# Kernel optimization log

Hardware: AMD Instinct MI355X
Metric: run time of the kernel (lower is better)

The kernel has to match this reference:

```python
import jax, jax.numpy as jnp
from jax import lax
import numpy as np

N = 20000        # nodes
E = 160000       # directed edges (doubled to 2E inside forward)
NODE_DIM = 6
EDGE_DIM = 4
HID = 64         # hidden_dim
HEADS = 4
ITERS = 3
D_OUT = HEADS * HID          # 256
SQRT_D = 8.0                 # sqrt(HID)
ALLOWED = jnp.array([8., 23., 39., 54., 90., 180.], dtype=jnp.float32)


def _ln(x, g, b):
    m = jnp.mean(x, -1, keepdims=True)
    v = jnp.mean((x - m) ** 2, -1, keepdims=True)
    return (x - m) * lax.rsqrt(v + 1e-5) * g + b


def _cbam(x, w1, b1, w2, b2, cw, cb):
    # channel attention: pool over nodes (dim 0)
    pool = jnp.concatenate([x.max(0, keepdims=True), x.mean(0, keepdims=True)], axis=1)  # [1,2D]
    ch = jax.nn.sigmoid(jnp.maximum(pool @ w1 + b1, 0.) @ w2 + b2)                        # [1,D]
    x = x * ch
    # spatial attention: pool over features, conv1d over node axis
    cat = jnp.concatenate([x.max(-1, keepdims=True), x.mean(-1, keepdims=True)], axis=-1)  # [N,2]
    inp = cat.T[None]                                                                       # [1,2,N]
    sp = lax.conv_general_dilated(inp, cw, (1,), [(3, 3)],
                                  dimension_numbers=('NCH', 'OIH', 'NCH')) + cb[None, :, None]
    return x * jax.nn.sigmoid(sp)[0, 0][:, None]


def _tconv(xc, src, dst, wq, b_q, wk, b_k, wv, b_v, ws, b_s):
    # PyG TransformerConv (concat=True, root_weight=True, no edge features)
    n = xc.shape[0]
    q = (xc @ wq + b_q).reshape(n, HEADS, HID)
    k = (xc @ wk + b_k).reshape(n, HEADS, HID)
    v = (xc @ wv + b_v).reshape(n, HEADS, HID)
    alpha = jnp.einsum('ehd,ehd->eh', q[dst], k[src]) / SQRT_D           # [2E,H]
    amax = jax.ops.segment_max(alpha, dst, num_segments=n)
    a = jnp.exp(alpha - amax[dst])
    a = a / jax.ops.segment_sum(a, dst, num_segments=n)[dst]
    out = jax.ops.segment_sum(a[..., None] * v[src], dst, num_segments=n).reshape(n, D_OUT)
    return out + xc @ ws + b_s


def reference(x, edge_attr, node_w, node_b, edge_w, edge_b, z_emb,
              cn_w1, cn_b1, cn_w2, cn_b2, cn_cw, cn_cb,
              ce_w1, ce_b1, ce_w2, ce_b2, ce_cw, ce_cb,
              Wq, bq, Wk, bk, Wv, bv, Ws, bs,
              lt_g, lt_b, lc_g, lc_b,
              pe_w, pe_b, pn_w, pn_b, gf_w, gf_b,
              c_w1, c_b1, c_w2, c_b2, edge_index):
    send = jnp.concatenate([edge_index[0], edge_index[1]])
    recv = jnp.concatenate([edge_index[1], edge_index[0]])
    src, dst = send, recv                                           # [2E]
    rel = x[src, :3] - x[dst, :3]                                   # [2E,3]
    zi = jnp.argmin(jnp.abs(jnp.round(x[:, 2])[:, None] - ALLOWED[None, :]), axis=1)
    nf = jnp.maximum(x @ node_w + node_b, 0.) + z_emb[zi]           # node embedding + z embedding
    nf = _cbam(nf, cn_w1, cn_b1, cn_w2, cn_b2, cn_cw, cn_cb)
    ef = jnp.concatenate([jnp.concatenate([edge_attr, edge_attr], 0), rel], axis=1)
    ef = jnp.maximum(ef @ edge_w + edge_b, 0.)
    ef = _cbam(ef, ce_w1, ce_b1, ce_w2, ce_b2, ce_cw, ce_cb)
    n = nf.shape[0]
    for i in range(ITERS):
        x0, e0 = nf, ef
        agg = jax.ops.segment_sum(ef, dst, num_segments=n)          # scatter-add messages
        comb = _ln(jnp.concatenate([nf, agg - nf], 1), lc_g[i], lc_b[i])
        out = _tconv(comb, src, dst, Wq[i], bq[i], Wk[i], bk[i], Wv[i], bv[i], Ws[i], bs[i])
        out = _ln(out, lt_g[i], lt_b[i])
        pn = out @ pn_w[i] + pn_b[i]
        g = jax.nn.sigmoid(jnp.concatenate([nf, pn], 1) @ gf_w[i] + gf_b[i])  # gated fusion
        nf = nf * g + pn * (1. - g)
        ef = (out[src] - out[dst]) @ pe_w[i] + pe_b[i]
        nf = nf + x0
        ef = ef + e0
    clf = jnp.concatenate([nf[edge_index[0]], nf[edge_index[1]]], axis=1)
    h = jnp.maximum(clf @ c_w1 + c_b1, 0.)
    return (h @ c_w2 + c_b2)[:, 0]


def setup_inputs() -> dict:
    key = jax.random.key(0)
    ki = iter(jax.random.split(key, 64))
    def rn(shape, s=0.05):
        return jax.random.normal(next(ki), shape, dtype=jnp.float32) * s
    x = jax.random.normal(next(ki), (N, NODE_DIM), dtype=jnp.float32)
    x = x.at[:, 2].set(ALLOWED[jax.random.randint(next(ki), (N,), 0, 6)])
    inp = {
        'x': x,
        'edge_attr': jax.random.normal(next(ki), (E, EDGE_DIM), dtype=jnp.float32),
        'node_w': rn((NODE_DIM, HID)), 'node_b': jnp.zeros(HID),
        'edge_w': rn((EDGE_DIM + 3, HID)), 'edge_b': jnp.zeros(HID),
        'z_emb': rn((6, HID)),
        'cn_w1': rn((2 * HID, HID // 16)), 'cn_b1': jnp.zeros(HID // 16),
        'cn_w2': rn((HID // 16, HID)), 'cn_b2': jnp.zeros(HID),
        'cn_cw': rn((1, 2, 7)), 'cn_cb': jnp.zeros(1),
        'ce_w1': rn((2 * HID, HID // 16)), 'ce_b1': jnp.zeros(HID // 16),
        'ce_w2': rn((HID // 16, HID)), 'ce_b2': jnp.zeros(HID),
        'ce_cw': rn((1, 2, 7)), 'ce_cb': jnp.zeros(1),
        'Wq': rn((ITERS, 2 * HID, D_OUT)), 'bq': jnp.zeros((ITERS, D_OUT)),
        'Wk': rn((ITERS, 2 * HID, D_OUT)), 'bk': jnp.zeros((ITERS, D_OUT)),
        'Wv': rn((ITERS, 2 * HID, D_OUT)), 'bv': jnp.zeros((ITERS, D_OUT)),
        'Ws': rn((ITERS, 2 * HID, D_OUT)), 'bs': jnp.zeros((ITERS, D_OUT)),
        'lt_g': jnp.ones((ITERS, D_OUT)), 'lt_b': jnp.zeros((ITERS, D_OUT)),
        'lc_g': jnp.ones((ITERS, 2 * HID)), 'lc_b': jnp.zeros((ITERS, 2 * HID)),
        'pe_w': rn((ITERS, D_OUT, HID)), 'pe_b': jnp.zeros((ITERS, HID)),
        'pn_w': rn((ITERS, D_OUT, HID)), 'pn_b': jnp.zeros((ITERS, HID)),
        'gf_w': rn((ITERS, 2 * HID, HID)), 'gf_b': jnp.zeros((ITERS, HID)),
        'c_w1': rn((2 * HID, HID)), 'c_b1': jnp.zeros(HID),
        'c_w2': rn((HID, 1)), 'c_b2': jnp.zeros(1),
        'edge_index': jax.random.randint(next(ki), (2, E), 0, N),
    }
    return inp
```

## Files before the change

kernel.cpp:

```cpp
#include <hip/hip_runtime.h>
#include <math.h>

typedef __attribute__((ext_vector_type(8))) short short8;
typedef __attribute__((ext_vector_type(4))) float f32x4;

__device__ __forceinline__ float wave_sum(float v){
  #pragma unroll
  for (int m = 32; m; m >>= 1) v += __shfl_xor(v, m, 64);
  return v;
}
__device__ __forceinline__ unsigned fenc(float f){
  unsigned u = __float_as_uint(f);
  return (u >> 31) ? ~u : (u | 0x80000000u);
}
__device__ __forceinline__ float fdec(unsigned e){
  return (e >> 31) ? __uint_as_float(e & 0x7fffffffu) : __uint_as_float(~e);
}
__device__ __forceinline__ float sigm(float x){ return 1.f / (1.f + __expf(-x)); }
__device__ __forceinline__ unsigned short f2bf(float f){
  union { float f; unsigned u; } x; x.f = f;
  unsigned r = x.u + 0x7fffu + ((x.u >> 16) & 1u);
  return (unsigned short)(r >> 16);
}
__device__ __forceinline__ float bf2f(unsigned short h){
  union { unsigned u; float f; } x; x.u = ((unsigned)h) << 16;
  return x.f;
}

__global__ void k_build_edges(const int* __restrict__ ei, int E2, int E,
                              int* __restrict__ src, int* __restrict__ dst,
                              int* __restrict__ deg){
  int e = blockIdx.x * blockDim.x + threadIdx.x;
  if (e >= E2) return;
  int s = ei[e];
  int d = (e < E) ? ei[e + E] : ei[e - E];
  src[e] = s; dst[e] = d;
  atomicAdd(&deg[d], 1);
}

__global__ void k_scan(const int* __restrict__ deg, int* __restrict__ rowptr, int N){
  __shared__ int part[1024];
  int t = threadIdx.x;
  int chunk = (N + 1023) / 1024;
  int lo = t * chunk, hi = lo + chunk; if (hi > N) hi = N;
  int s = 0;
  for (int i = lo; i < hi; ++i) s += deg[i];
  part[t] = s;
  __syncthreads();
  for (int off = 1; off < 1024; off <<= 1){
    int v = (t >= off) ? part[t - off] : 0;
    __syncthreads();
    part[t] += v;
    __syncthreads();
  }
  int run = part[t] - s;
  for (int i = lo; i < hi; ++i){ rowptr[i] = run; run += deg[i]; }
  if (t == 1023) rowptr[N] = part[1023];
}

__global__ void k_fill(const int* __restrict__ src, const int* __restrict__ dst,
                       const int* __restrict__ rowptr,
                       int* __restrict__ cur, int* __restrict__ csrc,
                       int* __restrict__ epos,
                       const float* __restrict__ x, const float* __restrict__ ea,
                       float* __restrict__ re8, int E2, int E){
  int e = blockIdx.x * blockDim.x + threadIdx.x;
  if (e >= E2) return;
  int s = src[e], d = dst[e];
  int pos = rowptr[d] + atomicAdd(&cur[d], 1);
  csrc[pos] = s;
  epos[e] = pos;
  int row = (e < E) ? e : e - E;
  float4 eav = *reinterpret_cast<const float4*>(ea + (size_t)row*4);
  float r0 = x[s*6]     - x[d*6];
  float r1 = x[s*6 + 1] - x[d*6 + 1];
  float r2 = x[s*6 + 2] - x[d*6 + 2];
  *reinterpret_cast<float4*>(re8 + (size_t)e*8)     = eav;
  *reinterpret_cast<float4*>(re8 + (size_t)e*8 + 4) = make_float4(r0, r1, r2, 0.f);
}

__global__ void k_embed_pool(const float* __restrict__ x, const float* __restrict__ nw,
                             const float* __restrict__ nb, const float* __restrict__ zemb,
                             float* __restrict__ nf,
                             unsigned* __restrict__ pmax, float* __restrict__ psum, int N){
  int tx = threadIdx.x & 63;
  int ty = threadIdx.x >> 6;
  const float allowed[6] = {8.f, 23.f, 39.f, 54.f, 90.f, 180.f};
  float m = -INFINITY, s = 0.f;
  for (int n = blockIdx.x*4 + ty; n < N; n += gridDim.x*4){
    float xv[6];
    #pragma unroll
    for (int k = 0; k < 6; ++k) xv[k] = x[n*6 + k];
    float v = nb[tx];
    #pragma unroll
    for (int k = 0; k < 6; ++k) v += xv[k] * nw[k*64 + tx];
    v = fmaxf(v, 0.f);
    float r = rintf(xv[2]);
    int zi = 0; float bd = fabsf(r - allowed[0]);
    #pragma unroll
    for (int k = 1; k < 6; ++k){ float d = fabsf(r - allowed[k]); if (d < bd){ bd = d; zi = k; } }
    v += zemb[zi*64 + tx];
    nf[(size_t)n*64 + tx] = v;
    m = fmaxf(m, v); s += v;
  }
  __shared__ float sm[4][64], ss[4][64];
  sm[ty][tx] = m; ss[ty][tx] = s;
  __syncthreads();
  if (ty == 0){
    #pragma unroll
    for (int k = 1; k < 4; ++k){ m = fmaxf(m, sm[k][tx]); s += ss[k][tx]; }
    atomicMax(&pmax[tx], fenc(m));
    atomicAdd(&psum[tx], s);
  }
}

__global__ void k_cbam_mlp(const unsigned* __restrict__ pmax, const float* __restrict__ psum,
                           float invR,
                           const float* __restrict__ w1, const float* __restrict__ b1,
                           const float* __restrict__ w2, const float* __restrict__ b2,
                           float* __restrict__ ch){
  __shared__ float pool[128];
  __shared__ float h[4];
  int t = threadIdx.x;
  pool[t]      = fdec(pmax[t]);
  pool[64 + t] = psum[t] * invR;
  __syncthreads();
  if (t < 4){
    float a = b1[t];
    for (int k = 0; k < 128; ++k) a += pool[k] * w1[k*4 + t];
    h[t] = fmaxf(a, 0.f);
  }
  __syncthreads();
  float a = b2[t];
  #pragma unroll
  for (int k = 0; k < 4; ++k) a += h[k] * w2[k*64 + t];
  ch[t] = sigm(a);
}

__global__ __launch_bounds__(256) void k_nsp(
    float* __restrict__ nf, const float* __restrict__ ch,
    const float* __restrict__ cw, const float* __restrict__ cb,
    unsigned short* __restrict__ gin, int N){
  __shared__ float s_v[134*65];
  __shared__ float s_rp[134][2];
  int tid = threadIdx.x;
  int tx = tid & 63, wv = tid >> 6;
  float chl = ch[tx];
  int base = blockIdx.x * 128;
  for (int li = wv; li < 134; li += 4){
    int r = base - 3 + li;
    if (r >= 0 && r < N)
      s_v[li*65 + tx] = nf[(size_t)r*64 + tx] * chl;
  }
  __syncthreads();
  #pragma unroll
  for (int pass = 0; pass < 2; ++pass){
    int li = (tid >> 1) + pass*128;
    if (li < 134){
      int r = base - 3 + li;
      if (r >= 0 && r < N){
        const float* vb = &s_v[li*65 + (tid & 1)*32];
        float m = vb[0], s = vb[0];
        #pragma unroll 8
        for (int k = 1; k < 32; ++k){ float t = vb[k]; m = fmaxf(m, t); s += t; }
        float mo = __shfl_xor(m, 1, 64);
        float so = __shfl_xor(s, 1, 64);
        m = fmaxf(m, mo); s += so;
        if ((tid & 1) == 0){ s_rp[li][0] = m; s_rp[li][1] = s * (1.f/64.f); }
      }
    }
  }
  __syncthreads();
  for (int li = 3 + wv; li < 131; li += 4){
    int r = base - 3 + li;
    if (r >= N) continue;
    float sp = cb[0];
    #pragma unroll
    for (int t7 = 0; t7 < 7; ++t7){
      int rr = r + t7 - 3;
      if (rr >= 0 && rr < N)
        sp += cw[t7] * s_rp[li - 3 + t7][0] + cw[7 + t7] * s_rp[li - 3 + t7][1];
    }
    float nfv = s_v[li*65 + tx] * sigm(sp);
    nf[(size_t)r*64 + tx] = nfv;
    gin[(size_t)r*128 + tx] = f2bf(nfv);
  }
}

__global__ __launch_bounds__(256) void k_ecol(
    const float* __restrict__ re8,
    const float* __restrict__ ew, const float* __restrict__ eb,
    unsigned* __restrict__ pmax, float* __restrict__ psum, int E2){
  __shared__ float s_re[2][1024];
  int tid = threadIdx.x;
  int tx = tid & 63, wv = tid >> 6;
  float ewr[7];
  #pragma unroll
  for (int k = 0; k < 7; ++k) ewr[k] = ew[k*64 + tx];
  float ebl = eb[tx];
  const int CHUNK = 128;
  int base0  = blockIdx.x * CHUNK;
  int stride = gridDim.x * CHUNK;
  float m = -INFINITY, s = 0.f;
  if (base0 < E2){
    int g0 = base0 * 8;
    #pragma unroll
    for (int q = 0; q < 4; ++q){
      int idx = q*256 + tid;
      int gi = g0 + idx;
      s_re[0][idx] = (gi < E2*8) ? re8[gi] : 0.f;
    }
  }
  int buf = 0;
  for (int base = base0; base < E2; base += stride){
    __syncthreads();
    int nb = base + stride;
    if (nb < E2){
      int g0 = nb * 8;
      #pragma unroll
      for (int q = 0; q < 4; ++q){
        int idx = q*256 + tid;
        int gi = g0 + idx;
        s_re[buf ^ 1][idx] = (gi < E2*8) ? re8[gi] : 0.f;
      }
    }
    const float* sb = s_re[buf];
    #pragma unroll
    for (int j = 0; j < 32; ++j){
      int e = base + wv*32 + j;
      if (e < E2){
        const float* r = &sb[(wv*32 + j)*8];
        float v = ebl;
        #pragma unroll
        for (int k = 0; k < 7; ++k) v += r[k] * ewr[k];
        v = fmaxf(v, 0.f);
        m = fmaxf(m, v); s += v;
      }
    }
    buf ^= 1;
  }
  __shared__ float sm[4][64], ss[4][64];
  sm[wv][tx] = m; ss[wv][tx] = s;
  __syncthreads();
  if (wv == 0){
    #pragma unroll
    for (int k = 1; k < 4; ++k){ m = fmaxf(m, sm[k][tx]); s += ss[k][tx]; }
    atomicMax(&pmax[tx], fenc(m));
    atomicAdd(&psum[tx], s);
  }
}

__global__ __launch_bounds__(256) void k_erp3(
    const float* __restrict__ re8, const int* __restrict__ epos,
    const float* __restrict__ ew, const float* __restrict__ eb,
    const float* __restrict__ ch,
    const float* __restrict__ ccw, const float* __restrict__ ccb,
    unsigned short* __restrict__ ef0, float* __restrict__ se, int E2){
  __shared__ float s_re[134*8];
  __shared__ float s_v[134*65];
  __shared__ float s_rp[134][2];
  __shared__ int   s_ep[128];
  int tid = threadIdx.x;
  int tx = tid & 63, wv = tid >> 6;
  float ewr[7];
  #pragma unroll
  for (int k = 0; k < 7; ++k) ewr[k] = ew[k*64 + tx];
  float ebl = eb[tx], chl = ch[tx];
  int base = blockIdx.x * 128;
  for (int idx = tid; idx < 134*8; idx += 256){
    int li = idx >> 3, k = idx & 7;
    int e = base - 3 + li;
    s_re[idx] = (e >= 0 && e < E2) ? re8[(size_t)e*8 + k] : 0.f;
  }
  if (tid < 128 && base + tid < E2) s_ep[tid] = epos[base + tid];
  __syncthreads();
  for (int li = wv; li < 134; li += 4){
    int e = base - 3 + li;
    if (e < 0 || e >= E2) continue;
    const float* r = &s_re[li*8];
    float v = ebl;
    #pragma unroll
    for (int k = 0; k < 7; ++k) v += r[k] * ewr[k];
    v = fmaxf(v, 0.f) * chl;
    s_v[li*65 + tx] = v;
    if (li >= 3 && li < 131)
      ef0[(size_t)s_ep[li - 3]*64 + tx] = f2bf(v);
  }
  __syncthreads();
  #pragma unroll
  for (int pass = 0; pass < 2; ++pass){
    int li = (tid >> 1) + pass*128;
    if (li < 134){
      int e = base - 3 + li;
      if (e >= 0 && e < E2){
        const float* vb = &s_v[li*65 + (tid & 1)*32];
        float m = vb[0], s = vb[0];
        #pragma unroll 8
        for (int k = 1; k < 32; ++k){ float t = vb[k]; m = fmaxf(m, t); s += t; }
        float mo = __shfl_xor(m, 1, 64);
        float so = __shfl_xor(s, 1, 64);
        m = fmaxf(m, mo); s += so;
        if ((tid & 1) == 0){ s_rp[li][0] = m; s_rp[li][1] = s * (1.f/64.f); }
      }
    }
  }
  __syncthreads();
  if (tid < 128){
    int e = base + tid;
    if (e < E2){
      float sp = ccb[0];
      #pragma unroll
      for (int t7 = 0; t7 < 7; ++t7){
        int rr = e + t7 - 3;
        if (rr >= 0 && rr < E2)
          sp += ccw[t7] * s_rp[tid + t7][0] + ccw[7 + t7] * s_rp[tid + t7][1];
      }
      se[s_ep[tid]] = sigm(sp);
    }
  }
}

__global__ void k_aggb(const unsigned short* __restrict__ ef0, const float* __restrict__ se,
                       const int* __restrict__ rowptr, const float* __restrict__ nf,
                       const float* __restrict__ g, const float* __restrict__ b,
                       float* __restrict__ agg, unsigned short* __restrict__ comb, int N){
  int n = blockIdx.x*4 + (threadIdx.x >> 6);
  if (n >= N) return;
  int l = threadIdx.x & 63;
  int lo = rowptr[n], hi = rowptr[n+1];
  float acc = 0.f;
  int i = lo;
  for (; i + 8 <= hi; i += 8){
    float sv[8], ev[8];
    #pragma unroll
    for (int j = 0; j < 8; ++j) sv[j] = se[i + j];
    #pragma unroll
    for (int j = 0; j < 8; ++j) ev[j] = bf2f(ef0[(size_t)(i + j)*64 + l]);
    #pragma unroll
    for (int j = 0; j < 8; ++j) acc += sv[j] * ev[j];
  }
  for (; i < hi; ++i) acc += se[i] * bf2f(ef0[(size_t)i*64 + l]);
  agg[(size_t)n*64 + l] = acc;
  float a = nf[(size_t)n*64 + l];
  float v0 = a, v1 = acc - a;
  float mean = wave_sum(v0 + v1) * (1.f/128.f);
  float d0 = v0 - mean, d1 = v1 - mean;
  float var = wave_sum(d0*d0 + d1*d1) * (1.f/128.f);
  float rs = rsqrtf(var + 1e-5f);
  comb[(size_t)n*128 + l]      = f2bf(d0 * rs * g[l]      + b[l]);
  comb[(size_t)n*128 + 64 + l] = f2bf(d1 * rs * g[64 + l] + b[64 + l]);
}

__global__ __launch_bounds__(256) void k_packT1(
    const float* __restrict__ Wq, const float* __restrict__ Wk,
    const float* __restrict__ Wv, const float* __restrict__ Ws,
    unsigned short* __restrict__ Bt){
  __shared__ float t[64][65];
  int bx = blockIdx.x, by = blockIdx.y, bz = blockIdx.z;
  const float* W = (bz == 0) ? Wq : (bz == 1) ? Wk : (bz == 2) ? Wv : Ws;
  int tx = threadIdx.x & 63, ty = threadIdx.x >> 6;
  int R0 = by*64, C0 = bx*64;
  for (int r = ty; r < 64; r += 4)
    t[r][tx] = W[(size_t)(R0 + r)*256 + C0 + tx];
  __syncthreads();
  int iter = by >> 1, kr0 = (by & 1)*64;
  for (int r = ty; r < 64; r += 4)
    Bt[(size_t)iter*1024*128 + (size_t)(bz*256 + C0 + r)*128 + kr0 + tx] = f2bf(t[tx][r]);
}

__global__ __launch_bounds__(256) void k_packT2(
    const float* __restrict__ Wn, const float* __restrict__ We,
    unsigned short* __restrict__ Bt2){
  __shared__ float t[64][65];
  int by = blockIdx.y, bz = blockIdx.z;
  const float* W = (bz == 0) ? Wn : We;
  int tx = threadIdx.x & 63, ty = threadIdx.x >> 6;
  int R0 = by*64;
  for (int r = ty; r < 64; r += 4)
    t[r][tx] = W[(size_t)(R0 + r)*64 + tx];
  __syncthreads();
  int iter = by >> 2, kr0 = (by & 3)*64;
  for (int r = ty; r < 64; r += 4)
    Bt2[(size_t)iter*128*256 + (size_t)(bz*64 + r)*256 + kr0 + tx] = f2bf(t[tx][r]);
}

__global__ void k_packG(const float* __restrict__ gfw, unsigned short* __restrict__ BtG){
  int b = blockIdx.x;
  int iter = b >> 7, col = b & 127;
  int k = threadIdx.x;
  unsigned short v = 0;
  if (col < 64) v = f2bf(gfw[(size_t)iter*128*64 + (size_t)k*64 + col]);
  BtG[(size_t)b*128 + k] = v;
}

__global__ void k_biasp(const float* __restrict__ bq, const float* __restrict__ bk,
                        const float* __restrict__ bv, const float* __restrict__ bs,
                        const float* __restrict__ pnb, const float* __restrict__ gfb,
                        float* __restrict__ bias, float* __restrict__ bias2,
                        float* __restrict__ bias3){
  int i = blockIdx.x, t = threadIdx.x;
  const float* bb = (t < 256) ? bq : (t < 512) ? bk : (t < 768) ? bv : bs;
  bias[i*1024 + t] = bb[i*256 + (t & 255)];
  if (t < 64){
    bias2[i*128 + t] = pnb[i*64 + t];
    bias3[i*128 + t] = gfb[i*64 + t];
  } else if (t < 128){
    bias2[i*128 + t] = 0.f;
    bias3[i*128 + t] = 0.f;
  }
}

__global__ void k_packC(const float* __restrict__ cw1, float* __restrict__ Wp){
  int idx = blockIdx.x * blockDim.x + threadIdx.x;
  if (idx >= 64*128) return;
  int k = idx >> 7, j = idx & 127;
  Wp[idx] = (j < 64) ? cw1[k*64 + j] : cw1[(64 + k)*64 + (j - 64)];
}

template<int NSTEPS, int MODE>
__global__ __launch_bounds__(256) void k_mfma(
    const unsigned short* __restrict__ A, int lda,
    const unsigned short* __restrict__ Bt, int ldb,
    const float* __restrict__ bias,
    float* __restrict__ o_f0, unsigned short* __restrict__ o_h0,
    unsigned short* __restrict__ o_h1, int M){
  __shared__ char ldsA[16384];
  int tid = threadIdx.x;
  int nbase = blockIdx.x * 128;
  int mbase = blockIdx.y * 64;
  int l = tid & 63, wid = tid >> 6;
  int wm = (wid & 1) * 32, wn = (wid >> 1) * 64;
  f32x4 acc[2][4] = {};
  const char* Ab  = (const char*)A;
  const char* Btb = (const char*)Bt;
  for (int ks = 0; ks < NSTEPS; ++ks){
    #pragma unroll
    for (int it = 0; it < 4; ++it){
      int c = tid + it*256;
      int row = c >> 4;
      int kb = (c & 15) << 4;
      int off = (row << 8) + (kb ^ ((row & 7) << 4));
      uint4 va = make_uint4(0,0,0,0);
      int gr = mbase + row;
      if (gr < M)
        va = *reinterpret_cast<const uint4*>(Ab + (size_t)gr*(lda*2) + ks*256 + kb);
      *reinterpret_cast<uint4*>(ldsA + off) = va;
    }
    __syncthreads();
    #pragma unroll
    for (int kk = 0; kk < 4; ++kk){
      int kbyte = kk*64 + (l >> 4)*16;
      short8 af[2], bf[4];
      #pragma unroll
      for (int n = 0; n < 4; ++n){
        int fc = wn + n*16 + (l & 15);
        bf[n] = *reinterpret_cast<const short8*>(
                  Btb + (size_t)(nbase + fc)*(ldb*2) + ks*256 + kbyte);
      }
      #pragma unroll
      for (int m = 0; m < 2; ++m){
        int fr = wm + m*16 + (l & 15);
        af[m] = *reinterpret_cast<const short8*>(ldsA + (fr << 8) + (kbyte ^ ((fr & 7) << 4)));
      }
      #pragma unroll
      for (int m = 0; m < 2; ++m)
        #pragma unroll
        for (int n = 0; n < 4; ++n)
          acc[m][n] = __builtin_amdgcn_mfma_f32_16x16x32_bf16(af[m], bf[n], acc[m][n], 0, 0, 0);
    }
    __syncthreads();
  }
  #pragma unroll
  for (int n = 0; n < 4; ++n){
    int gcol = nbase + wn + n*16 + (l & 15);
    float bv = bias ? bias[gcol] : 0.f;
    #pragma unroll
    for (int m = 0; m < 2; ++m){
      int grow = mbase + wm + m*16 + (l >> 4)*4;
      #pragma unroll
      for (int r = 0; r < 4; ++r){
        int gr = grow + r;
        if (gr < M){
          float val = acc[m][n][r] + bv;
          if (MODE == 1){
            o_f0[(size_t)gr*128 + gcol] = val;
            if (gcol < 64) o_h0[(size_t)gr*128 + 64 + gcol] = f2bf(val);
          } else if (MODE == 2){
            if (gcol < 64) o_f0[(size_t)gr*64 + gcol] = val;
          } else {
            int seg = gcol >> 8, c = gcol & 255;
            if      (seg == 0) o_h1[(size_t)gr*512 + c] = f2bf(val);
            else if (seg == 1) o_h0[(size_t)gr*512 + c] = f2bf(val);
            else if (seg == 2) o_h0[(size_t)gr*512 + 256 + c] = f2bf(val);
            else               o_h1[(size_t)gr*512 + 256 + c] = f2bf(val);
          }
        }
      }
    }
  }
}

__global__ void k_attn(const unsigned short* __restrict__ qs,
                       const unsigned short* __restrict__ kv,
                       const int* __restrict__ rowptr, const int* __restrict__ csrc,
                       const float* __restrict__ ltg, const float* __restrict__ ltb,
                       unsigned short* __restrict__ outb, int N){
  int n = blockIdx.x*4 + (threadIdx.x >> 6);
  if (n >= N) return;
  int l = threadIdx.x & 63;
  int lo = rowptr[n], hi = rowptr[n+1];
  const int l4 = l*4;
  ushort4 qu = *reinterpret_cast<const ushort4*>(qs + (size_t)n*512 + l4);
  float4 qv = make_float4(bf2f(qu.x)*0.125f, bf2f(qu.y)*0.125f,
                          bf2f(qu.z)*0.125f, bf2f(qu.w)*0.125f);
  float o0 = 0.f, o1 = 0.f, o2 = 0.f, o3 = 0.f, s = 0.f;
  int i = lo;
  for (; i + 16 <= hi; i += 16){
    ushort4 kk[16], vv[16];
    #pragma unroll
    for (int j = 0; j < 16; ++j){
      const unsigned short* row = kv + (size_t)csrc[i + j]*512 + l4;
      kk[j] = *reinterpret_cast<const ushort4*>(row);
      vv[j] = *reinterpret_cast<const ushort4*>(row + 256);
    }
    float a[16];
    #pragma unroll
    for (int j = 0; j < 16; ++j)
      a[j] = qv.x*bf2f(kk[j].x) + qv.y*bf2f(kk[j].y) + qv.z*bf2f(kk[j].z) + qv.w*bf2f(kk[j].w);
    #pragma unroll
    for (int m = 1; m < 16; m <<= 1){
      #pragma unroll
      for (int j = 0; j < 16; ++j) a[j] += __shfl_xor(a[j], m, 64);
    }
    #pragma unroll
    for (int j = 0; j < 16; ++j){
      float w = __expf(a[j]);
      s += w;
      o0 += w*bf2f(vv[j].x); o1 += w*bf2f(vv[j].y);
      o2 += w*bf2f(vv[j].z); o3 += w*bf2f(vv[j].w);
    }
  }
  for (; i + 8 <= hi; i += 8){
    ushort4 kk[8], vv[8];
    #pragma unroll
    for (int j = 0; j < 8; ++j){
      const unsigned short* row = kv + (size_t)csrc[i + j]*512 + l4;
      kk[j] = *reinterpret_cast<const ushort4*>(row);
      vv[j] = *reinterpret_cast<const ushort4*>(row + 256);
    }
    float a[8];
    #pragma unroll
    for (int j = 0; j < 8; ++j)
      a[j] = qv.x*bf2f(kk[j].x) + qv.y*bf2f(kk[j].y) + qv.z*bf2f(kk[j].z) + qv.w*bf2f(kk[j].w);
    #pragma unroll
    for (int m = 1; m < 16; m <<= 1){
      #pragma unroll
      for (int j = 0; j < 8; ++j) a[j] += __shfl_xor(a[j], m, 64);
    }
    #pragma unroll
    for (int j = 0; j < 8; ++j){
      float w = __expf(a[j]);
      s += w;
      o0 += w*bf2f(vv[j].x); o1 += w*bf2f(vv[j].y);
      o2 += w*bf2f(vv[j].z); o3 += w*bf2f(vv[j].w);
    }
  }
  for (; i < hi; ++i){
    const unsigned short* row = kv + (size_t)csrc[i]*512 + l4;
    ushort4 kk = *reinterpret_cast<const ushort4*>(row);
    ushort4 vv = *reinterpret_cast<const ushort4*>(row + 256);
    float a = qv.x*bf2f(kk.x) + qv.y*bf2f(kk.y) + qv.z*bf2f(kk.z) + qv.w*bf2f(kk.w);
    #pragma unroll
    for (int m = 1; m < 16; m <<= 1) a += __shfl_xor(a, m, 64);
    float w = __expf(a);
    s += w;
    o0 += w*bf2f(vv.x); o1 += w*bf2f(vv.y); o2 += w*bf2f(vv.z); o3 += w*bf2f(vv.w);
  }
  ushort4 su = *reinterpret_cast<const ushort4*>(qs + (size_t)n*512 + 256 + l4);
  float tx0 = bf2f(su.x), tx1 = bf2f(su.y), tx2 = bf2f(su.z), tx3 = bf2f(su.w);
  if (hi > lo){
    float r = 1.f / s;
    tx0 += o0*r; tx1 += o1*r; tx2 += o2*r; tx3 += o3*r;
  }
  float mean = wave_sum(tx0 + tx1 + tx2 + tx3) * (1.f/256.f);
  float dx = tx0 - mean, dy = tx1 - mean, dz = tx2 - mean, dw = tx3 - mean;
  float var = wave_sum(dx*dx + dy*dy + dz*dz + dw*dw) * (1.f/256.f);
  float rs = rsqrtf(var + 1e-5f);
  float4 g = *reinterpret_cast<const float4*>(ltg + l4);
  float4 b = *reinterpret_cast<const float4*>(ltb + l4);
  ushort4 o;
  o.x = f2bf(dx*rs*g.x + b.x);
  o.y = f2bf(dy*rs*g.y + b.y);
  o.z = f2bf(dz*rs*g.z + b.z);
  o.w = f2bf(dw*rs*g.w + b.w);
  *reinterpret_cast<ushort4*>(outb + (size_t)n*256 + l4) = o;
}

__global__ __launch_bounds__(256) void k_gate2(
    float* __restrict__ nf, float* __restrict__ agg,
    const float* __restrict__ pnP, const float* __restrict__ gate_arg,
    const int* __restrict__ rowptr, const int* __restrict__ csrc,
    const float* __restrict__ peb,
    const float* __restrict__ cg, const float* __restrict__ cbv,
    unsigned short* __restrict__ comb, unsigned short* __restrict__ gin,
    int doComb, int N){
  int n = blockIdx.x*4 + (threadIdx.x >> 6);
  if (n >= N) return;
  int l = threadIdx.x & 63;
  float g = sigm(gate_arg[(size_t)n*64 + l]);
  float nfv = nf[(size_t)n*64 + l];
  float pnv = pnP[(size_t)n*128 + l];
  float nfn = nfv * (1.f + g) + pnv * (1.f - g);
  nf[(size_t)n*64 + l] = nfn;
  gin[(size_t)n*128 + l] = f2bf(nfn);
  int lo = rowptr[n], hi = rowptr[n+1];
  float sp = 0.f;
  int i = lo;
  for (; i + 8 <= hi; i += 8){
    float pv[8];
    #pragma unroll
    for (int j = 0; j < 8; ++j)
      pv[j] = pnP[(size_t)csrc[i+j]*128 + 64 + l];
    #pragma unroll
    for (int j = 0; j < 8; ++j) sp += pv[j];
  }
  for (; i < hi; ++i) sp += pnP[(size_t)csrc[i]*128 + 64 + l];
  float Pn = pnP[(size_t)n*128 + 64 + l];
  float aggn = agg[(size_t)n*64 + l] + sp - (float)(hi - lo) * (Pn - peb[l]);
  agg[(size_t)n*64 + l] = aggn;
  if (doComb){
    float v0 = nfn, v1 = aggn - nfn;
    float mean = wave_sum(v0 + v1) * (1.f/128.f);
    float d0 = v0 - mean, d1 = v1 - mean;
    float var = wave_sum(d0*d0 + d1*d1) * (1.f/128.f);
    float rs = rsqrtf(var + 1e-5f);
    comb[(size_t)n*128 + l]      = f2bf(d0 * rs * cg[l]      + cbv[l]);
    comb[(size_t)n*128 + 64 + l] = f2bf(d1 * rs * cg[64 + l] + cbv[64 + l]);
  }
}

template<int K, int BN>
__global__ __launch_bounds__(256) void k_gemm(
    const float* __restrict__ in, const float* __restrict__ W, int ldw,
    const float* __restrict__ bias, float* __restrict__ out, int ldo, int nrows){
  constexpr int PAD = BN + 4;
  __shared__ float s_in[K * PAD];
  int n0 = blockIdx.x * BN;
  int tid = threadIdx.x;
  for (int idx = tid; idx < BN * K; idx += 256){
    int r = idx / K, k = idx - r * K;
    float v = (n0 + r < nrows) ? in[(size_t)(n0 + r) * K + k] : 0.f;
    s_in[k * PAD + r] = v;
  }
  __syncthreads();
  int tx = tid & 15, ty = tid >> 4;
  constexpr int NT = BN / 16;
  int col0 = blockIdx.y * 64 + tx * 4;
  float acc[NT][4] = {};
  for (int k = 0; k < K; ++k){
    const float4 wv = *reinterpret_cast<const float4*>(&W[(size_t)k * ldw + col0]);
    #pragma unroll
    for (int i = 0; i < NT; ++i){
      float cv = s_in[k * PAD + ty * NT + i];
      acc[i][0] += cv * wv.x;
      acc[i][1] += cv * wv.y;
      acc[i][2] += cv * wv.z;
      acc[i][3] += cv * wv.w;
    }
  }
  #pragma unroll
  for (int i = 0; i < NT; ++i){
    int n = n0 + ty * NT + i;
    if (n < nrows){
      float4 o = make_float4(acc[i][0], acc[i][1], acc[i][2], acc[i][3]);
      *reinterpret_cast<float4*>(&out[(size_t)n * ldo + col0]) = o;
    }
  }
}

__global__ void k_final(const float* __restrict__ AB,
                        const int* __restrict__ ei, const float* __restrict__ cb1,
                        const float* __restrict__ cw2, const float* __restrict__ cb2,
                        float* __restrict__ dout, int E){
  int e = blockIdx.x*4 + (threadIdx.x >> 6);
  if (e >= E) return;
  int l = threadIdx.x & 63;
  int i0 = ei[e], i1 = ei[E + e];
  float h = fmaxf(AB[(size_t)i0*128 + l] + AB[(size_t)i1*128 + 64 + l] + cb1[l], 0.f);
  float p = wave_sum(h * cw2[l]);
  if (l == 0) dout[e] = p + cb2[0];
}

extern "C" void kernel_launch(void* const* d_in, const int* in_sizes, int n_in,
                              void* d_out, int out_size, void* d_ws, size_t ws_size,
                              hipStream_t stream){
  const float* x         = (const float*)d_in[0];
  const float* edge_attr = (const float*)d_in[1];
  const float* node_w    = (const float*)d_in[2];
  const float* node_b    = (const float*)d_in[3];
  const float* edge_w    = (const float*)d_in[4];
  const float* edge_b    = (const float*)d_in[5];
  const float* z_emb     = (const float*)d_in[6];
  const float* cn_w1     = (const float*)d_in[7];
  const float* cn_b1     = (const float*)d_in[8];
  const float* cn_w2     = (const float*)d_in[9];
  const float* cn_b2     = (const float*)d_in[10];
  const float* cn_cw     = (const float*)d_in[11];
  const float* cn_cb     = (const float*)d_in[12];
  const float* ce_w1     = (const float*)d_in[13];
  const float* ce_b1     = (const float*)d_in[14];
  const float* ce_w2     = (const float*)d_in[15];
  const float* ce_b2     = (const float*)d_in[16];
  const float* ce_cw     = (const float*)d_in[17];
  const float* ce_cb     = (const float*)d_in[18];
  const float* Wq        = (const float*)d_in[19];
  const float* bq        = (const float*)d_in[20];
  const float* Wk        = (const float*)d_in[21];
  const float* bk        = (const float*)d_in[22];
  const float* Wv        = (const float*)d_in[23];
  const float* bv        = (const float*)d_in[24];
  const float* Ws        = (const float*)d_in[25];
  const float* bs        = (const float*)d_in[26];
  const float* lt_g      = (const float*)d_in[27];
  const float* lt_b      = (const float*)d_in[28];
  const float* lc_g      = (const float*)d_in[29];
  const float* lc_b      = (const float*)d_in[30];
  const float* pe_w      = (const float*)d_in[31];
  const float* pe_b      = (const float*)d_in[32];
  const float* pn_w      = (const float*)d_in[33];
  const float* pn_b      = (const float*)d_in[34];
  const float* gf_w      = (const float*)d_in[35];
  const float* gf_b      = (const float*)d_in[36];
  const float* c_w1      = (const float*)d_in[37];
  const float* c_b1      = (const float*)d_in[38];
  const float* c_w2      = (const float*)d_in[39];
  const float* c_b2      = (const float*)d_in[40];
  const int*   edge_index= (const int*)d_in[41];

  const int N  = in_sizes[0] / 6;
  const int E  = in_sizes[1] / 4;
  const int E2 = 2 * E;

  char* p = (char*)d_ws;
  auto alloc = [&](size_t bytes)->char*{
    char* r = p; p += (bytes + 255) & ~(size_t)255; return r;
  };
  char* zbase = p;
  int*            w_deg    = (int*)           alloc((size_t)N * 4);
  int*            w_cur    = (int*)           alloc((size_t)N * 4);
  unsigned*       w_pmax   = (unsigned*)      alloc(64 * 4);
  float*          w_psum   = (float*)         alloc(64 * 4);
  unsigned*       w_pmax2  = (unsigned*)      alloc(64 * 4);
  float*          w_psum2  = (float*)         alloc(64 * 4);
  size_t zbytes = (size_t)(p - zbase);
  int*            w_src    = (int*)           alloc((size_t)E2 * 4);
  int*            w_dst    = (int*)           alloc((size_t)E2 * 4);
  int*            w_rowptr = (int*)           alloc((size_t)(N + 1) * 4);
  int*            w_csrc   = (int*)           alloc((size_t)E2 * 4);
  int*            w_epos   = (int*)           alloc((size_t)E2 * 4);
  float*          w_re8    = (float*)         alloc((size_t)E2 * 8 * 4);
  float*          w_nf     = (float*)         alloc((size_t)N * 64 * 4);
  float*          w_agg    = (float*)         alloc((size_t)N * 64 * 4);
  unsigned short* w_ef0    = (unsigned short*)alloc((size_t)E2 * 64 * 2);
  float*          w_se     = (float*)         alloc((size_t)E2 * 4);
  unsigned short* w_comb   = (unsigned short*)alloc((size_t)N * 128 * 2);
  unsigned short* w_gin    = (unsigned short*)alloc((size_t)N * 128 * 2);
  float*          w_gate   = (float*)         alloc((size_t)N * 64 * 4);
  unsigned short* w_qs     = (unsigned short*)alloc((size_t)N * 512 * 2);
  unsigned short* w_kv     = (unsigned short*)alloc((size_t)N * 512 * 2);
  unsigned short* w_outb   = (unsigned short*)alloc((size_t)N * 256 * 2);
  float*          w_pnP    = (float*)         alloc((size_t)N * 128 * 4);
  float*          w_AB     = (float*)         alloc((size_t)N * 128 * 4);
  float*          w_Wp     = (float*)         alloc((size_t)64 * 128 * 4);
  unsigned short* w_Bt     = (unsigned short*)alloc((size_t)3 * 1024 * 128 * 2);
  float*          w_bias   = (float*)         alloc((size_t)3 * 1024 * 4);
  unsigned short* w_Bt2    = (unsigned short*)alloc((size_t)3 * 128 * 256 * 2);
  float*          w_bias2  = (float*)         alloc((size_t)3 * 128 * 4);
  unsigned short* w_BtG    = (unsigned short*)alloc((size_t)3 * 128 * 128 * 2);
  float*          w_bias3  = (float*)         alloc((size_t)3 * 128 * 4);
  float*          w_ch     = (float*)         alloc(64 * 4);
  float*          w_ch2    = (float*)         alloc(64 * 4);

  hipMemsetAsync(zbase, 0, zbytes, stream);

  k_build_edges<<<(E2 + 255)/256, 256, 0, stream>>>(edge_index, E2, E, w_src, w_dst, w_deg);
  k_scan<<<1, 1024, 0, stream>>>(w_deg, w_rowptr, N);
  k_fill<<<(E2 + 255)/256, 256, 0, stream>>>(w_src, w_dst, w_rowptr, w_cur, w_csrc, w_epos,
                                             x, edge_attr, w_re8, E2, E);
  k_embed_pool<<<256, 256, 0, stream>>>(x, node_w, node_b, z_emb, w_nf, w_pmax, w_psum, N);
  k_cbam_mlp<<<1, 64, 0, stream>>>(w_pmax, w_psum, 1.f/(float)N,
                                   cn_w1, cn_b1, cn_w2, cn_b2, w_ch);
  k_nsp<<<(N + 127)/128, 256, 0, stream>>>(w_nf, w_ch, cn_cw, cn_cb, w_gin, N);

  k_ecol<<<256, 256, 0, stream>>>(w_re8, edge_w, edge_b, w_pmax2, w_psum2, E2);
  k_cbam_mlp<<<1, 64, 0, stream>>>(w_pmax2, w_psum2, 1.f/(float)E2,
                                   ce_w1, ce_b1, ce_w2, ce_b2, w_ch2);
  k_erp3<<<(E2 + 127)/128, 256, 0, stream>>>(w_re8, w_epos, edge_w, edge_b, w_ch2,
                                             ce_cw, ce_cb, w_ef0, w_se, E2);
  k_aggb<<<(N + 3)/4, 256, 0, stream>>>(w_ef0, w_se, w_rowptr, w_nf,
                                        lc_g, lc_b, w_agg, w_comb, N);

  k_packT1<<<dim3(4, 6, 4), 256, 0, stream>>>(Wq, Wk, Wv, Ws, w_Bt);
  k_packT2<<<dim3(1, 12, 2), 256, 0, stream>>>(pn_w, pe_w, w_Bt2);
  k_packG<<<3*128, 128, 0, stream>>>(gf_w, w_BtG);
  k_biasp<<<3, 1024, 0, stream>>>(bq, bk, bv, bs, pn_b, gf_b, w_bias, w_bias2, w_bias3);
  k_packC<<<32, 256, 0, stream>>>(c_w1, w_Wp);

  const int MB2 = (N + 63) / 64;
  for (int i = 0; i < 3; ++i){
    k_mfma<1,0><<<dim3(8, MB2), 256, 0, stream>>>(w_comb, 128,
                                                  w_Bt + (size_t)i*1024*128, 128,
                                                  w_bias + (size_t)i*1024,
                                                  nullptr, w_kv, w_qs, N);
    k_attn<<<(N + 3)/4, 256, 0, stream>>>(w_qs, w_kv, w_rowptr, w_csrc,
                                          lt_g + (size_t)i*256, lt_b + (size_t)i*256,
                                          w_outb, N);
    k_mfma<2,1><<<dim3(1, MB2), 256, 0, stream>>>(w_outb, 256,
                                                  w_Bt2 + (size_t)i*128*256, 256,
                                                  w_bias2 + (size_t)i*128,
                                                  w_pnP, w_gin, nullptr, N);
    k_mfma<1,2><<<dim3(1, MB2), 256, 0, stream>>>(w_gin, 128,
                                                  w_BtG + (size_t)i*128*128, 128,
                                                  w_bias3 + (size_t)i*128,
                                                  w_gate, nullptr, nullptr, N);
    int doComb = (i < 2) ? 1 : 0;
    const float* cg  = lc_g + (size_t)(i < 2 ? i+1 : 0)*128;
    const float* cbv = lc_b + (size_t)(i < 2 ? i+1 : 0)*128;
    k_gate2<<<(N + 3)/4, 256, 0, stream>>>(w_nf, w_agg, w_pnP, w_gate,
                                           w_rowptr, w_csrc,
                                           pe_b + (size_t)i*64,
                                           cg, cbv, w_comb, w_gin, doComb, N);
  }

  dim3 gAB((N + 63)/64, 2);
  k_gemm<64,64><<<gAB, 256, 0, stream>>>(w_nf, w_Wp, 128, nullptr, w_AB, 128, N);
  k_final<<<(E + 3)/4, 256, 0, stream>>>(w_AB, edge_index, c_b1, c_w2, c_b2,
                                         (float*)d_out, E);
}
```

Measured before the change: 710.4 us.

## Gather neighbor projections from compact bf16 copy; drop 16-edge attention unroll

The MODE 1 GEMM epilogue now also writes the second 64 columns of the projection as a compact bf16 array. The gate kernel's neighbor-sum gather reads that array instead of strided fp32 rows, which cuts gather traffic per edge. Separately, the 16-wide unrolled edge loop in the attention kernel is removed, leaving the 8-wide loop, to lower register pressure and raise occupancy. The bf16 gather adds rounding error to the aggregate, and the smaller unroll has fewer loads in flight per wave.

Measured after the change: 692.1 us. 2.6% less time.

```diff
diff --git a/kernel.cpp b/kernel.cpp
--- a/kernel.cpp
+++ b/kernel.cpp
@@ -485,6 +485,7 @@
           if (MODE == 1){
             o_f0[(size_t)gr*128 + gcol] = val;
             if (gcol < 64) o_h0[(size_t)gr*128 + 64 + gcol] = f2bf(val);
+            else           o_h1[(size_t)gr*64 + (gcol - 64)] = f2bf(val);
           } else if (MODE == 2){
             if (gcol < 64) o_f0[(size_t)gr*64 + gcol] = val;
           } else {
@@ -515,31 +516,6 @@
                           bf2f(qu.z)*0.125f, bf2f(qu.w)*0.125f);
   float o0 = 0.f, o1 = 0.f, o2 = 0.f, o3 = 0.f, s = 0.f;
   int i = lo;
-  for (; i + 16 <= hi; i += 16){
-    ushort4 kk[16], vv[16];
-    #pragma unroll
-    for (int j = 0; j < 16; ++j){
-      const unsigned short* row = kv + (size_t)csrc[i + j]*512 + l4;
-      kk[j] = *reinterpret_cast<const ushort4*>(row);
-      vv[j] = *reinterpret_cast<const ushort4*>(row + 256);
-    }
-    float a[16];
-    #pragma unroll
-    for (int j = 0; j < 16; ++j)
-      a[j] = qv.x*bf2f(kk[j].x) + qv.y*bf2f(kk[j].y) + qv.z*bf2f(kk[j].z) + qv.w*bf2f(kk[j].w);
-    #pragma unroll
-    for (int m = 1; m < 16; m <<= 1){
-      #pragma unroll
-      for (int j = 0; j < 16; ++j) a[j] += __shfl_xor(a[j], m, 64);
-    }
-    #pragma unroll
-    for (int j = 0; j < 16; ++j){
-      float w = __expf(a[j]);
-      s += w;
-      o0 += w*bf2f(vv[j].x); o1 += w*bf2f(vv[j].y);
-      o2 += w*bf2f(vv[j].z); o3 += w*bf2f(vv[j].w);
-    }
-  }
   for (; i + 8 <= hi; i += 8){
     ushort4 kk[8], vv[8];
     #pragma unroll
@@ -598,7 +574,8 @@
 
 __global__ __launch_bounds__(256) void k_gate2(
     float* __restrict__ nf, float* __restrict__ agg,
-    const float* __restrict__ pnP, const float* __restrict__ gate_arg,
+    const float* __restrict__ pnP, const unsigned short* __restrict__ Pbf,
+    const float* __restrict__ gate_arg,
     const int* __restrict__ rowptr, const int* __restrict__ csrc,
     const float* __restrict__ peb,
     const float* __restrict__ cg, const float* __restrict__ cbv,
@@ -620,12 +597,12 @@
     float pv[8];
     #pragma unroll
     for (int j = 0; j < 8; ++j)
-      pv[j] = pnP[(size_t)csrc[i+j]*128 + 64 + l];
+      pv[j] = bf2f(Pbf[(size_t)csrc[i+j]*64 + l]);
     #pragma unroll
     for (int j = 0; j < 8; ++j) sp += pv[j];
   }
-  for (; i < hi; ++i) sp += pnP[(size_t)csrc[i]*128 + 64 + l];
-  float Pn = pnP[(size_t)n*128 + 64 + l];
+  for (; i < hi; ++i) sp += bf2f(Pbf[(size_t)csrc[i]*64 + l]);
+  float Pn = bf2f(Pbf[(size_t)n*64 + l]);
   float aggn = agg[(size_t)n*64 + l] + sp - (float)(hi - lo) * (Pn - peb[l]);
   agg[(size_t)n*64 + l] = aggn;
   if (doComb){
@@ -770,6 +747,7 @@
   unsigned short* w_kv     = (unsigned short*)alloc((size_t)N * 512 * 2);
   unsigned short* w_outb   = (unsigned short*)alloc((size_t)N * 256 * 2);
   float*          w_pnP    = (float*)         alloc((size_t)N * 128 * 4);
+  unsigned short* w_Pbf    = (unsigned short*)alloc((size_t)N * 64 * 2);
   float*          w_AB     = (float*)         alloc((size_t)N * 128 * 4);
   float*          w_Wp     = (float*)         alloc((size_t)64 * 128 * 4);
   unsigned short* w_Bt     = (unsigned short*)alloc((size_t)3 * 1024 * 128 * 2);
@@ -818,7 +796,7 @@
     k_mfma<2,1><<<dim3(1, MB2), 256, 0, stream>>>(w_outb, 256,
                                                   w_Bt2 + (size_t)i*128*256, 256,
                                                   w_bias2 + (size_t)i*128,
-                                                  w_pnP, w_gin, nullptr, N);
+                                                  w_pnP, w_gin, w_Pbf, N);
     k_mfma<1,2><<<dim3(1, MB2), 256, 0, stream>>>(w_gin, 128,
                                                   w_BtG + (size_t)i*128*128, 128,
                                                   w_bias3 + (size_t)i*128,
@@ -826,7 +804,7 @@
     int doComb = (i < 2) ? 1 : 0;
     const float* cg  = lc_g + (size_t)(i < 2 ? i+1 : 0)*128;
     const float* cbv = lc_b + (size_t)(i < 2 ? i+1 : 0)*128;
-    k_gate2<<<(N + 3)/4, 256, 0, stream>>>(w_nf, w_agg, w_pnP, w_gate,
+    k_gate2<<<(N + 3)/4, 256, 0, stream>>>(w_nf, w_agg, w_pnP, w_Pbf, w_gate,
                                            w_rowptr, w_csrc,
                                            pe_b + (size_t)i*64,
                                            cg, cbv, w_comb, w_gin, doComb, N);
```
